# Optimization experiments

Hardware: AMD Instinct MI355X
Metric: run time of the kernel (lower is better)

## Reference

```python
import jax, jax.numpy as jnp
import numpy as np

N, D, E = 50000, 64, 800000  # nodes, node_dim, edges


def setup_inputs() -> dict:
    key = jax.random.key(0)
    ks = jax.random.split(key, 9)
    def lin(kw, fan_in, fan_out):
        # torch nn.Linear default init: U(-1/sqrt(fan_in), 1/sqrt(fan_in))
        bound = 1.0 / np.sqrt(fan_in)
        kw1, kw2 = jax.random.split(kw)
        W = jax.random.uniform(kw1, (fan_in, fan_out), jnp.float32, -bound, bound)
        b = jax.random.uniform(kw2, (fan_out,), jnp.float32, -bound, bound)
        return W, b
    W1, b1 = lin(ks[0], 2 * D + 2, D)
    W2, b2 = lin(ks[1], D, D // 2)
    W3, b3 = lin(ks[2], D // 2, D // 4)
    return {
        "node_features": jax.random.normal(ks[3], (N, D), jnp.float32),
        "edge_index": jax.random.randint(ks[4], (2, E), 0, N, jnp.int64),
        "spatial_features": jax.random.normal(ks[5], (E, 2), jnp.float32),
        "W1": W1, "b1": b1, "W2": W2, "b2": b2, "W3": W3, "b3": b3,
    }


def reference(node_features, edge_index, spatial_features, W1, b1, W2, b2, W3, b3):
    src = node_features[edge_index[0]]          # [E, D] gather
    dst = node_features[edge_index[1]]          # [E, D] gather
    x = jnp.concatenate([src, dst, spatial_features], axis=1)  # [E, 2D+2]
    h = jax.nn.relu(x @ W1 + b1)                # [E, D]
    h = jax.nn.relu(h @ W2 + b2)                # [E, D//2]
    return h @ W3 + b3                          # [E, D//4]
```

## Files before the change

kernel.cpp:

```cpp
#include <hip/hip_runtime.h>
#include <hip/hip_bf16.h>

#define NE 800000
#define NN 50000
#define TPW 5
#define NTILES (NE / 16)
#define NODE_TILES (NN / 16)
#define W1STR 136

typedef __attribute__((ext_vector_type(8))) short        s16x8;
typedef __attribute__((ext_vector_type(4))) short        s16x4;
typedef __attribute__((ext_vector_type(8))) __bf16       bf16x8;
typedef __attribute__((ext_vector_type(4))) __bf16       bf16x4;
typedef __attribute__((ext_vector_type(4))) float        f32x4;
typedef __attribute__((ext_vector_type(2))) float        f32x2;
typedef __attribute__((ext_vector_type(4))) unsigned int u32x4;
typedef __attribute__((ext_vector_type(2))) unsigned int u32x2;

#define TAB_OFF 16384
#define WS_TAB ((size_t)(TAB_OFF + 2ull * NN * 64) * 2)
#define WS_NFB ((size_t)(TAB_OFF + 1ull * NN * 64) * 2)

__device__ __forceinline__ unsigned short f2bf_bits(float f) {
    __bf16 b = (__bf16)f;
    return __builtin_bit_cast(unsigned short, b);
}

__device__ __forceinline__ unsigned int pkbf(float a, float b) {
    return (unsigned int)f2bf_bits(a) | ((unsigned int)f2bf_bits(b) << 16);
}

__device__ __forceinline__ s16x8 cvt8(f32x4 a, f32x4 b) {
    bf16x8 r;
    r[0] = (__bf16)a[0]; r[1] = (__bf16)a[1]; r[2] = (__bf16)a[2]; r[3] = (__bf16)a[3];
    r[4] = (__bf16)b[0]; r[5] = (__bf16)b[1]; r[6] = (__bf16)b[2]; r[7] = (__bf16)b[3];
    return __builtin_bit_cast(s16x8, r);
}

__device__ __forceinline__ int w1addr(int k, int j) {
    return j * W1STR + (((k >> 3) ^ ((j >> 2) & 15)) << 3) + (k & 7);
}

__global__ __launch_bounds__(256) void node_prep_all(
    const float* __restrict__ nf, const float* __restrict__ W1,
    const float* __restrict__ b1, const float* __restrict__ W2,
    const float* __restrict__ W3, unsigned short* __restrict__ ws) {
    unsigned short* w2t = ws + 10240;
    unsigned short* w3t = ws + 12288;
    unsigned short* At  = ws + TAB_OFF;
    unsigned short* Bt  = At + (size_t)NN * 64;

    __shared__ unsigned short w1l[64 * W1STR];

    const int tid = threadIdx.x, wid = tid >> 6, lane = tid & 63;
    const int lr = lane & 15, lg = lane >> 4;

    #pragma unroll
    for (int it = 0; it < 8; ++it) {
        const int i = it * 1024 + tid * 4;
        const int k = i >> 6, j0 = i & 63;
        f32x4 v = *reinterpret_cast<const f32x4*>(W1 + i);
        #pragma unroll
        for (int q = 0; q < 4; ++q)
            w1l[w1addr(k, j0 + q)] = f2bf_bits(v[q]);
    }
    __syncthreads();

    if (blockIdx.x == 0) {
        for (int i = tid; i < 32 * 64; i += 256) {
            int j = i / 64, k = i % 64;
            w2t[i] = f2bf_bits(W2[k * 32 + j]);
        }
        for (int i = tid; i < 16 * 32; i += 256) {
            int j = i / 32, k = i % 32;
            w3t[i] = f2bf_bits(W3[k * 16 + j]);
        }
    }

    s16x8 w1f[4][4];
    #pragma unroll
    for (int s = 0; s < 4; ++s)
        #pragma unroll
        for (int c = 0; c < 4; ++c)
            w1f[s][c] = *reinterpret_cast<const s16x8*>(
                &w1l[w1addr(s * 32 + lg * 8, c * 16 + lr)]);

    f32x4 b1q[4];
    #pragma unroll
    for (int c = 0; c < 4; ++c)
        b1q[c] = *reinterpret_cast<const f32x4*>(b1 + c * 16 + lg * 4);

    const int tile = blockIdx.x * 4 + wid;
    if (tile >= NODE_TILES) return;

    const int row = tile * 16 + lr;
    const float* p = nf + (long)row * 64;
    s16x8 nfr[2];
    #pragma unroll
    for (int s = 0; s < 2; ++s) {
        f32x4 a = *reinterpret_cast<const f32x4*>(p + s * 32 + lg * 8);
        f32x4 b = *reinterpret_cast<const f32x4*>(p + s * 32 + lg * 8 + 4);
        nfr[s] = cvt8(a, b);
    }
    f32x4 a4[4], b4[4];
    #pragma unroll
    for (int c = 0; c < 4; ++c) { a4[c] = (f32x4){0,0,0,0}; b4[c] = (f32x4){0,0,0,0}; }
    #pragma unroll
    for (int s = 0; s < 2; ++s)
        #pragma unroll
        for (int c = 0; c < 4; ++c) {
            a4[c] = __builtin_amdgcn_mfma_f32_16x16x32_bf16(w1f[s][c],     nfr[s], a4[c], 0, 0, 0);
            b4[c] = __builtin_amdgcn_mfma_f32_16x16x32_bf16(w1f[s + 2][c], nfr[s], b4[c], 0, 0, 0);
        }
    #pragma unroll
    for (int c = 0; c < 4; ++c) {
        u32x2 pa, pb;
        pa[0] = pkbf(a4[c][0] + b1q[c][0], a4[c][1] + b1q[c][1]);
        pa[1] = pkbf(a4[c][2] + b1q[c][2], a4[c][3] + b1q[c][3]);
        pb[0] = pkbf(b4[c][0], b4[c][1]);
        pb[1] = pkbf(b4[c][2], b4[c][3]);
        *reinterpret_cast<u32x2*>(At + (long)row * 64 + c * 16 + lg * 4) = pa;
        *reinterpret_cast<u32x2*>(Bt + (long)row * 64 + c * 16 + lg * 4) = pb;
    }
}

__device__ __forceinline__ void gatherT(const unsigned short* At, const unsigned short* Bt,
                                        int si, int di, int lg, s16x8 g[4]) {
    const unsigned short* pa = At + (size_t)si * 64 + lg * 8;
    const unsigned short* pb = Bt + (size_t)di * 64 + lg * 8;
    g[0] = *reinterpret_cast<const s16x8*>(pa);
    g[1] = *reinterpret_cast<const s16x8*>(pa + 32);
    g[2] = *reinterpret_cast<const s16x8*>(pb);
    g[3] = *reinterpret_cast<const s16x8*>(pb + 32);
}

__device__ __forceinline__ void compute_tile(
    int tile, const s16x8 cur[4], f32x2 s2,
    const f32x2 c0p[2][4], const f32x2 c1p[2][4],
    const s16x8 w2f[2][2], s16x8 w3f,
    const f32x4 b2v[2], f32x4 b3v,
    unsigned short* h2w, int lg, int lr, float* __restrict__ out) {

    const f32x2 sp0v = {s2[0], s2[0]}, sp1v = {s2[1], s2[1]};

    s16x8 bfr[2];
    #pragma unroll
    for (int jb = 0; jb < 2; ++jb) {
        u32x4 au = __builtin_bit_cast(u32x4, cur[jb]);
        u32x4 bu = __builtin_bit_cast(u32x4, cur[2 + jb]);
        u32x4 pk4;
        #pragma unroll
        for (int q = 0; q < 4; ++q) {
            f32x2 av = {__builtin_bit_cast(float, au[q] << 16),
                        __builtin_bit_cast(float, au[q] & 0xFFFF0000u)};
            f32x2 bv = {__builtin_bit_cast(float, bu[q] << 16),
                        __builtin_bit_cast(float, bu[q] & 0xFFFF0000u)};
            f32x2 h = av + bv;
            h = sp1v * c1p[jb][q] + h;
            h = sp0v * c0p[jb][q] + h;
            pk4[q] = pkbf(fmaxf(h[0], 0.f), fmaxf(h[1], 0.f));
        }
        bfr[jb] = __builtin_bit_cast(s16x8, pk4);
    }

    f32x4 acc2[2];
    #pragma unroll
    for (int c = 0; c < 2; ++c) acc2[c] = (f32x4){0, 0, 0, 0};
    #pragma unroll
    for (int s = 0; s < 2; ++s)
        #pragma unroll
        for (int c = 0; c < 2; ++c)
            acc2[c] = __builtin_amdgcn_mfma_f32_16x16x32_bf16(w2f[s][c], bfr[s], acc2[c], 0, 0, 0);

    #pragma unroll
    for (int c = 0; c < 2; ++c) {
        u32x2 p;
        p[0] = pkbf(fmaxf(acc2[c][0] + b2v[c][0], 0.f), fmaxf(acc2[c][1] + b2v[c][1], 0.f));
        p[1] = pkbf(fmaxf(acc2[c][2] + b2v[c][2], 0.f), fmaxf(acc2[c][3] + b2v[c][3], 0.f));
        *reinterpret_cast<u32x2*>(h2w + c * 16 + lg * 4) = p;
    }

    s16x8 bf3 = *reinterpret_cast<const s16x8*>(h2w + lg * 8);
    f32x4 acc3 = (f32x4){0, 0, 0, 0};
    acc3 = __builtin_amdgcn_mfma_f32_16x16x32_bf16(w3f, bf3, acc3, 0, 0, 0);

    f32x4 o;
    #pragma unroll
    for (int r = 0; r < 4; ++r) o[r] = acc3[r] + b3v[r];
    __builtin_nontemporal_store(o,
        reinterpret_cast<f32x4*>(out + (long)(tile * 16 + lr) * 16 + lg * 4));
}

__global__ __launch_bounds__(256) void edge_mlp_tab(
    const int* __restrict__ ei, const float* __restrict__ sp,
    const float* __restrict__ W1, const float* __restrict__ b2,
    const float* __restrict__ b3, const unsigned short* __restrict__ wsw,
    float* __restrict__ out) {

    const unsigned short* w2t = wsw + 10240;
    const unsigned short* w3t = wsw + 12288;
    const unsigned short* At  = wsw + TAB_OFF;
    const unsigned short* Bt  = At + (size_t)NN * 64;

    __shared__ unsigned short h2s[4 * 16 * 40];

    const int tid = threadIdx.x, wid = tid >> 6, lane = tid & 63;
    const int lr = lane & 15, lg = lane >> 4;

    const int tile0 = (blockIdx.x * 4 + wid) * TPW;

    s16x8 w2f[2][2], w3f;
    #pragma unroll
    for (int s = 0; s < 2; ++s)
        #pragma unroll
        for (int c = 0; c < 2; ++c)
            w2f[s][c] = *reinterpret_cast<const s16x8*>(w2t + (c * 16 + lr) * 64 + s * 32 + lg * 8);
    w3f = *reinterpret_cast<const s16x8*>(w3t + lr * 32 + lg * 8);

    f32x4 b2v[2];
    #pragma unroll
    for (int c = 0; c < 2; ++c) b2v[c] = *reinterpret_cast<const f32x4*>(b2 + c * 16 + lg * 4);
    const f32x4 b3v = *reinterpret_cast<const f32x4*>(b3 + lg * 4);

    f32x2 c0p[2][4], c1p[2][4];
    #pragma unroll
    for (int jb = 0; jb < 2; ++jb) {
        const int j0 = jb * 32 + lg * 8;
        f32x4 x0 = *reinterpret_cast<const f32x4*>(W1 + 128 * 64 + j0);
        f32x4 x1 = *reinterpret_cast<const f32x4*>(W1 + 128 * 64 + j0 + 4);
        f32x4 y0 = *reinterpret_cast<const f32x4*>(W1 + 129 * 64 + j0);
        f32x4 y1 = *reinterpret_cast<const f32x4*>(W1 + 129 * 64 + j0 + 4);
        c0p[jb][0] = (f32x2){x0[0], x0[1]}; c0p[jb][1] = (f32x2){x0[2], x0[3]};
        c0p[jb][2] = (f32x2){x1[0], x1[1]}; c0p[jb][3] = (f32x2){x1[2], x1[3]};
        c1p[jb][0] = (f32x2){y0[0], y0[1]}; c1p[jb][1] = (f32x2){y0[2], y0[3]};
        c1p[jb][2] = (f32x2){y1[0], y1[1]}; c1p[jb][3] = (f32x2){y1[2], y1[3]};
    }

    unsigned short* h2w = h2s + wid * (16 * 40) + lr * 40;

    int si[TPW], di[TPW];
    f32x2 spv[TPW];
    #pragma unroll
    for (int t = 0; t < TPW; ++t) {
        const size_t e = (size_t)(tile0 + t) * 16 + lr;
        si[t] = ei[e];
        di[t] = ei[NE + e];
        spv[t] = *reinterpret_cast<const f32x2*>(sp + 2 * e);
    }

    s16x8 gA[4], gB[4], gC[4];
    gatherT(At, Bt, si[0], di[0], lg, gA);
    gatherT(At, Bt, si[1], di[1], lg, gB);

    gatherT(At, Bt, si[2], di[2], lg, gC);
    compute_tile(tile0 + 0, gA, spv[0], c0p, c1p, w2f, w3f, b2v, b3v, h2w, lg, lr, out);

    gatherT(At, Bt, si[3], di[3], lg, gA);
    compute_tile(tile0 + 1, gB, spv[1], c0p, c1p, w2f, w3f, b2v, b3v, h2w, lg, lr, out);

    gatherT(At, Bt, si[4], di[4], lg, gB);
    compute_tile(tile0 + 2, gC, spv[2], c0p, c1p, w2f, w3f, b2v, b3v, h2w, lg, lr, out);

    compute_tile(tile0 + 3, gA, spv[3], c0p, c1p, w2f, w3f, b2v, b3v, h2w, lg, lr, out);
    compute_tile(tile0 + 4, gB, spv[4], c0p, c1p, w2f, w3f, b2v, b3v, h2w, lg, lr, out);
}

__global__ void prep(const float* __restrict__ W1, const float* __restrict__ W2,
                     const float* __restrict__ W3, const float* __restrict__ nf,
                     unsigned short* __restrict__ ws, int do_nf) {
    unsigned short* w1t = ws;
    unsigned short* w2t = ws + 10240;
    unsigned short* w3t = ws + 12288;
    int t = blockIdx.x * blockDim.x + threadIdx.x;
    int stride = gridDim.x * blockDim.x;
    for (int i = t; i < 64 * 160; i += stride) {
        int j = i / 160, k = i % 160;
        w1t[i] = f2bf_bits(k < 130 ? W1[k * 64 + j] : 0.0f);
    }
    for (int i = t; i < 32 * 64; i += stride) {
        int j = i / 64, k = i % 64;
        w2t[i] = f2bf_bits(W2[k * 32 + j]);
    }
    for (int i = t; i < 16 * 32; i += stride) {
        int j = i / 32, k = i % 32;
        w3t[i] = f2bf_bits(W3[k * 16 + j]);
    }
    if (do_nf) {
        unsigned short* nfb = ws + TAB_OFF;
        for (int i = t; i < NN * 8; i += stride) {
            f32x4 a = *reinterpret_cast<const f32x4*>(nf + (long)i * 8);
            f32x4 b = *reinterpret_cast<const f32x4*>(nf + (long)i * 8 + 4);
            *reinterpret_cast<s16x8*>(nfb + (long)i * 8) = cvt8(a, b);
        }
    }
}

template <bool BF16NF>
__device__ __forceinline__ void gather4(const unsigned short* nfb, const float* nf,
                                        int si, int di, int lg, s16x8 g[4]) {
    if (BF16NF) {
        #pragma unroll
        for (int s = 0; s < 4; ++s) {
            const int row = (s < 2) ? si : di;
            g[s] = *reinterpret_cast<const s16x8*>(nfb + (long)row * 64 + (s & 1) * 32 + lg * 8);
        }
    } else {
        #pragma unroll
        for (int s = 0; s < 4; ++s) {
            const float* p = nf + (long)((s < 2) ? si : di) * 64 + (s & 1) * 32 + lg * 8;
            f32x4 a = *reinterpret_cast<const f32x4*>(p);
            f32x4 b = *reinterpret_cast<const f32x4*>(p + 4);
            g[s] = cvt8(a, b);
        }
    }
}

template <bool BF16NF>
__global__ __launch_bounds__(256) void edge_mlp_fb(
    const float* __restrict__ nf, const int* __restrict__ ei,
    const float* __restrict__ sp, const float* __restrict__ b1,
    const float* __restrict__ b2, const float* __restrict__ b3,
    const unsigned short* __restrict__ wsw, float* __restrict__ out) {

    const unsigned short* w1t = wsw;
    const unsigned short* w2t = wsw + 10240;
    const unsigned short* w3t = wsw + 12288;
    const unsigned short* nfb = wsw + TAB_OFF;

    __shared__ float h1s[4][16][68];
    __shared__ float h2s[4][16][36];

    const int tid = threadIdx.x, wid = tid >> 6, lane = tid & 63;
    const int lr = lane & 15, lg = lane >> 4;

    s16x8 w1f[5][4], w2f[2][2], w3f;
    #pragma unroll
    for (int s = 0; s < 5; ++s)
        #pragma unroll
        for (int c = 0; c < 4; ++c)
            w1f[s][c] = *reinterpret_cast<const s16x8*>(w1t + (c * 16 + lr) * 160 + s * 32 + lg * 8);
    #pragma unroll
    for (int s = 0; s < 2; ++s)
        #pragma unroll
        for (int c = 0; c < 2; ++c)
            w2f[s][c] = *reinterpret_cast<const s16x8*>(w2t + (c * 16 + lr) * 64 + s * 32 + lg * 8);
    w3f = *reinterpret_cast<const s16x8*>(w3t + lr * 32 + lg * 8);

    float bias1[4], bias2[2], bias3;
    #pragma unroll
    for (int c = 0; c < 4; ++c) bias1[c] = b1[c * 16 + lr];
    #pragma unroll
    for (int c = 0; c < 2; ++c) bias2[c] = b2[c * 16 + lr];
    bias3 = b3[lr];

    const int tile0 = (blockIdx.x * 4 + wid) * 4;
    int si[4], di[4];
    f32x2 spv[4];
    #pragma unroll
    for (int t = 0; t < 4; ++t) {
        const int e = (tile0 + t) * 16 + lr;
        si[t] = ei[e];
        di[t] = ei[NE + e];
        spv[t] = *reinterpret_cast<const f32x2*>(sp + 2 * (size_t)e);
    }

    s16x8 cur[4], nxt[4];
    gather4<BF16NF>(nfb, nf, si[0], di[0], lg, cur);

    #pragma unroll
    for (int tt = 0; tt < 4; ++tt) {
        if (tt + 1 < 4)
            gather4<BF16NF>(nfb, nf, si[tt + 1], di[tt + 1], lg, nxt);

        const int ebase = (tile0 + tt) * 16;

        f32x4 acc1[4];
        #pragma unroll
        for (int c = 0; c < 4; ++c) acc1[c] = (f32x4){0, 0, 0, 0};
        #pragma unroll
        for (int s = 0; s < 4; ++s)
            #pragma unroll
            for (int c = 0; c < 4; ++c)
                acc1[c] = __builtin_amdgcn_mfma_f32_16x16x32_bf16(cur[s], w1f[s][c], acc1[c], 0, 0, 0);
        {
            bf16x8 z;
            #pragma unroll
            for (int j = 0; j < 8; ++j) z[j] = (__bf16)0.0f;
            if (lg == 0) { z[0] = (__bf16)spv[tt][0]; z[1] = (__bf16)spv[tt][1]; }
            s16x8 af = __builtin_bit_cast(s16x8, z);
            #pragma unroll
            for (int c = 0; c < 4; ++c)
                acc1[c] = __builtin_amdgcn_mfma_f32_16x16x32_bf16(af, w1f[4][c], acc1[c], 0, 0, 0);
        }
        #pragma unroll
        for (int c = 0; c < 4; ++c)
            #pragma unroll
            for (int r = 0; r < 4; ++r)
                h1s[wid][lg * 4 + r][c * 16 + lr] = fmaxf(acc1[c][r] + bias1[c], 0.0f);

        f32x4 acc2[2];
        #pragma unroll
        for (int c = 0; c < 2; ++c) acc2[c] = (f32x4){0, 0, 0, 0};
        #pragma unroll
        for (int s = 0; s < 2; ++s) {
            f32x4 a = *reinterpret_cast<const f32x4*>(&h1s[wid][lr][s * 32 + lg * 8]);
            f32x4 b = *reinterpret_cast<const f32x4*>(&h1s[wid][lr][s * 32 + lg * 8 + 4]);
            s16x8 af = cvt8(a, b);
            #pragma unroll
            for (int c = 0; c < 2; ++c)
                acc2[c] = __builtin_amdgcn_mfma_f32_16x16x32_bf16(af, w2f[s][c], acc2[c], 0, 0, 0);
        }
        #pragma unroll
        for (int c = 0; c < 2; ++c)
            #pragma unroll
            for (int r = 0; r < 4; ++r)
                h2s[wid][lg * 4 + r][c * 16 + lr] = fmaxf(acc2[c][r] + bias2[c], 0.0f);

        f32x4 a3 = *reinterpret_cast<const f32x4*>(&h2s[wid][lr][lg * 8]);
        f32x4 b3x = *reinterpret_cast<const f32x4*>(&h2s[wid][lr][lg * 8 + 4]);
        s16x8 af3 = cvt8(a3, b3x);
        f32x4 acc3 = (f32x4){0, 0, 0, 0};
        acc3 = __builtin_amdgcn_mfma_f32_16x16x32_bf16(af3, w3f, acc3, 0, 0, 0);
        #pragma unroll
        for (int r = 0; r < 4; ++r)
            out[(long)(ebase + lg * 4 + r) * 16 + lr] = acc3[r] + bias3;

        #pragma unroll
        for (int s = 0; s < 4; ++s) cur[s] = nxt[s];
    }
}

extern "C" void kernel_launch(void* const* d_in, const int* in_sizes, int n_in,
                              void* d_out, int out_size, void* d_ws, size_t ws_size,
                              hipStream_t stream) {
    const float* nf = (const float*)d_in[0];
    const int*   ei = (const int*)d_in[1];
    const float* sp = (const float*)d_in[2];
    const float* W1 = (const float*)d_in[3];
    const float* b1 = (const float*)d_in[4];
    const float* W2 = (const float*)d_in[5];
    const float* b2 = (const float*)d_in[6];
    const float* W3 = (const float*)d_in[7];
    const float* b3 = (const float*)d_in[8];
    float* out = (float*)d_out;
    unsigned short* wsw = (unsigned short*)d_ws;

    const bool tab  = (ws_size >= WS_TAB);
    const bool bnfb = (!tab && ws_size >= WS_NFB);

    if (tab) {
        const int pblocks = (NODE_TILES + 3) / 4;
        hipLaunchKernelGGL(node_prep_all, dim3(pblocks), dim3(256), 0, stream,
                           nf, W1, b1, W2, W3, wsw);
        const int blocks = NTILES / (TPW * 4);
        hipLaunchKernelGGL(edge_mlp_tab, dim3(blocks), dim3(256), 0, stream,
                           ei, sp, W1, b2, b3, wsw, out);
    } else {
        hipLaunchKernelGGL(prep, dim3(64), dim3(256), 0, stream,
                           W1, W2, W3, nf, wsw, bnfb ? 1 : 0);
        const int blocks = NTILES / 4 / 4;
        if (bnfb)
            hipLaunchKernelGGL(edge_mlp_fb<true>, dim3(blocks), dim3(256), 0, stream,
                               nf, ei, sp, b1, b2, b3, wsw, out);
        else
            hipLaunchKernelGGL(edge_mlp_fb<false>, dim3(blocks), dim3(256), 0, stream,
                               nf, ei, sp, b1, b2, b3, wsw, out);
    }
}
```

Measured before the change: 57.08 us.

## Fuse node prep and edge MLP into one cooperative persistent kernel

Combines the node-table precompute and the edge MLP into a single cooperative kernel of 2048 blocks that uses a grid-wide sync between the two phases. This removes one kernel launch and the gap between launches. It also switches the edge phase to a persistent layout of 6 tiles per wave, with a tail tile for some waves and triple-buffered gathers. The cost is a grid barrier, occupancy checks on the host on every call, and register pressure from launch bounds of 8 blocks per CU.

```diff
diff --git a/kernel.cpp b/kernel.cpp
--- a/kernel.cpp
+++ b/kernel.cpp
@@ -1,5 +1,8 @@
 #include <hip/hip_runtime.h>
 #include <hip/hip_bf16.h>
+#include <hip/hip_cooperative_groups.h>
+
+namespace cg = cooperative_groups;
 
 #define NE 800000
 #define NN 50000
@@ -8,10 +11,13 @@
 #define NODE_TILES (NN / 16)
 #define W1STR 136
 
+#define FBLOCKS 2048
+#define FWAVES  (FBLOCKS * 4)
+#define FTPW    6
+#define FTAIL   (NTILES - FWAVES * FTPW)
+
 typedef __attribute__((ext_vector_type(8))) short        s16x8;
-typedef __attribute__((ext_vector_type(4))) short        s16x4;
 typedef __attribute__((ext_vector_type(8))) __bf16       bf16x8;
-typedef __attribute__((ext_vector_type(4))) __bf16       bf16x4;
 typedef __attribute__((ext_vector_type(4))) float        f32x4;
 typedef __attribute__((ext_vector_type(2))) float        f32x2;
 typedef __attribute__((ext_vector_type(4))) unsigned int u32x4;
@@ -39,89 +45,6 @@
 
 __device__ __forceinline__ int w1addr(int k, int j) {
     return j * W1STR + (((k >> 3) ^ ((j >> 2) & 15)) << 3) + (k & 7);
-}
-
-__global__ __launch_bounds__(256) void node_prep_all(
-    const float* __restrict__ nf, const float* __restrict__ W1,
-    const float* __restrict__ b1, const float* __restrict__ W2,
-    const float* __restrict__ W3, unsigned short* __restrict__ ws) {
-    unsigned short* w2t = ws + 10240;
-    unsigned short* w3t = ws + 12288;
-    unsigned short* At  = ws + TAB_OFF;
-    unsigned short* Bt  = At + (size_t)NN * 64;
-
-    __shared__ unsigned short w1l[64 * W1STR];
-
-    const int tid = threadIdx.x, wid = tid >> 6, lane = tid & 63;
-    const int lr = lane & 15, lg = lane >> 4;
-
-    #pragma unroll
-    for (int it = 0; it < 8; ++it) {
-        const int i = it * 1024 + tid * 4;
-        const int k = i >> 6, j0 = i & 63;
-        f32x4 v = *reinterpret_cast<const f32x4*>(W1 + i);
-        #pragma unroll
-        for (int q = 0; q < 4; ++q)
-            w1l[w1addr(k, j0 + q)] = f2bf_bits(v[q]);
-    }
-    __syncthreads();
-
-    if (blockIdx.x == 0) {
-        for (int i = tid; i < 32 * 64; i += 256) {
-            int j = i / 64, k = i % 64;
-            w2t[i] = f2bf_bits(W2[k * 32 + j]);
-        }
-        for (int i = tid; i < 16 * 32; i += 256) {
-            int j = i / 32, k = i % 32;
-            w3t[i] = f2bf_bits(W3[k * 16 + j]);
-        }
-    }
-
-    s16x8 w1f[4][4];
-    #pragma unroll
-    for (int s = 0; s < 4; ++s)
-        #pragma unroll
-        for (int c = 0; c < 4; ++c)
-            w1f[s][c] = *reinterpret_cast<const s16x8*>(
-                &w1l[w1addr(s * 32 + lg * 8, c * 16 + lr)]);
-
-    f32x4 b1q[4];
-    #pragma unroll
-    for (int c = 0; c < 4; ++c)
-        b1q[c] = *reinterpret_cast<const f32x4*>(b1 + c * 16 + lg * 4);
-
-    const int tile = blockIdx.x * 4 + wid;
-    if (tile >= NODE_TILES) return;
-
-    const int row = tile * 16 + lr;
-    const float* p = nf + (long)row * 64;
-    s16x8 nfr[2];
-    #pragma unroll
-    for (int s = 0; s < 2; ++s) {
-        f32x4 a = *reinterpret_cast<const f32x4*>(p + s * 32 + lg * 8);
-        f32x4 b = *reinterpret_cast<const f32x4*>(p + s * 32 + lg * 8 + 4);
-        nfr[s] = cvt8(a, b);
-    }
-    f32x4 a4[4], b4[4];
-    #pragma unroll
-    for (int c = 0; c < 4; ++c) { a4[c] = (f32x4){0,0,0,0}; b4[c] = (f32x4){0,0,0,0}; }
-    #pragma unroll
-    for (int s = 0; s < 2; ++s)
-        #pragma unroll
-        for (int c = 0; c < 4; ++c) {
-            a4[c] = __builtin_amdgcn_mfma_f32_16x16x32_bf16(w1f[s][c],     nfr[s], a4[c], 0, 0, 0);
-            b4[c] = __builtin_amdgcn_mfma_f32_16x16x32_bf16(w1f[s + 2][c], nfr[s], b4[c], 0, 0, 0);
-        }
-    #pragma unroll
-    for (int c = 0; c < 4; ++c) {
-        u32x2 pa, pb;
-        pa[0] = pkbf(a4[c][0] + b1q[c][0], a4[c][1] + b1q[c][1]);
-        pa[1] = pkbf(a4[c][2] + b1q[c][2], a4[c][3] + b1q[c][3]);
-        pb[0] = pkbf(b4[c][0], b4[c][1]);
-        pb[1] = pkbf(b4[c][2], b4[c][3]);
-        *reinterpret_cast<u32x2*>(At + (long)row * 64 + c * 16 + lg * 4) = pa;
-        *reinterpret_cast<u32x2*>(Bt + (long)row * 64 + c * 16 + lg * 4) = pb;
-    }
 }
 
 __device__ __forceinline__ void gatherT(const unsigned short* At, const unsigned short* Bt,
@@ -189,6 +112,251 @@
     for (int r = 0; r < 4; ++r) o[r] = acc3[r] + b3v[r];
     __builtin_nontemporal_store(o,
         reinterpret_cast<f32x4*>(out + (long)(tile * 16 + lr) * 16 + lg * 4));
+}
+
+__global__ __launch_bounds__(256, 8) void fused_all(
+    const float* __restrict__ nf, const int* __restrict__ ei,
+    const float* __restrict__ sp, const float* __restrict__ W1,
+    const float* __restrict__ b1, const float* __restrict__ W2,
+    const float* __restrict__ b2, const float* __restrict__ W3,
+    const float* __restrict__ b3, unsigned short* __restrict__ ws,
+    float* __restrict__ out) {
+
+    unsigned short* w2t = ws + 10240;
+    unsigned short* w3t = ws + 12288;
+    unsigned short* At  = ws + TAB_OFF;
+    unsigned short* Bt  = At + (size_t)NN * 64;
+
+    __shared__ unsigned short smem[64 * W1STR];
+
+    const int tid = threadIdx.x, wid = tid >> 6, lane = tid & 63;
+    const int lr = lane & 15, lg = lane >> 4;
+    const int gw = blockIdx.x * 4 + wid;
+
+    if (blockIdx.x < (NODE_TILES + 3) / 4) {
+        #pragma unroll
+        for (int it = 0; it < 8; ++it) {
+            const int i = it * 1024 + tid * 4;
+            const int k = i >> 6, j0 = i & 63;
+            f32x4 v = *reinterpret_cast<const f32x4*>(W1 + i);
+            #pragma unroll
+            for (int q = 0; q < 4; ++q)
+                smem[w1addr(k, j0 + q)] = f2bf_bits(v[q]);
+        }
+        __syncthreads();
+
+        if (blockIdx.x == 0) {
+            for (int i = tid; i < 32 * 64; i += 256) {
+                int j = i / 64, k = i % 64;
+                w2t[i] = f2bf_bits(W2[k * 32 + j]);
+            }
+            for (int i = tid; i < 16 * 32; i += 256) {
+                int j = i / 32, k = i % 32;
+                w3t[i] = f2bf_bits(W3[k * 16 + j]);
+            }
+        }
+
+        s16x8 w1f[4][4];
+        #pragma unroll
+        for (int s = 0; s < 4; ++s)
+            #pragma unroll
+            for (int c = 0; c < 4; ++c)
+                w1f[s][c] = *reinterpret_cast<const s16x8*>(
+                    &smem[w1addr(s * 32 + lg * 8, c * 16 + lr)]);
+
+        if (gw < NODE_TILES) {
+            f32x4 b1q[4];
+            #pragma unroll
+            for (int c = 0; c < 4; ++c)
+                b1q[c] = *reinterpret_cast<const f32x4*>(b1 + c * 16 + lg * 4);
+
+            const int row = gw * 16 + lr;
+            const float* p = nf + (long)row * 64;
+            s16x8 nfr[2];
+            #pragma unroll
+            for (int s = 0; s < 2; ++s) {
+                f32x4 a = *reinterpret_cast<const f32x4*>(p + s * 32 + lg * 8);
+                f32x4 b = *reinterpret_cast<const f32x4*>(p + s * 32 + lg * 8 + 4);
+                nfr[s] = cvt8(a, b);
+            }
+            f32x4 a4[4], b4[4];
+            #pragma unroll
+            for (int c = 0; c < 4; ++c) { a4[c] = (f32x4){0,0,0,0}; b4[c] = (f32x4){0,0,0,0}; }
+            #pragma unroll
+            for (int s = 0; s < 2; ++s)
+                #pragma unroll
+                for (int c = 0; c < 4; ++c) {
+                    a4[c] = __builtin_amdgcn_mfma_f32_16x16x32_bf16(w1f[s][c],     nfr[s], a4[c], 0, 0, 0);
+                    b4[c] = __builtin_amdgcn_mfma_f32_16x16x32_bf16(w1f[s + 2][c], nfr[s], b4[c], 0, 0, 0);
+                }
+            #pragma unroll
+            for (int c = 0; c < 4; ++c) {
+                u32x2 pa, pb;
+                pa[0] = pkbf(a4[c][0] + b1q[c][0], a4[c][1] + b1q[c][1]);
+                pa[1] = pkbf(a4[c][2] + b1q[c][2], a4[c][3] + b1q[c][3]);
+                pb[0] = pkbf(b4[c][0], b4[c][1]);
+                pb[1] = pkbf(b4[c][2], b4[c][3]);
+                *reinterpret_cast<u32x2*>(At + (long)row * 64 + c * 16 + lg * 4) = pa;
+                *reinterpret_cast<u32x2*>(Bt + (long)row * 64 + c * 16 + lg * 4) = pb;
+            }
+        }
+    }
+
+    __threadfence();
+    cg::this_grid().sync();
+
+    s16x8 w2f[2][2], w3f;
+    #pragma unroll
+    for (int s = 0; s < 2; ++s)
+        #pragma unroll
+        for (int c = 0; c < 2; ++c)
+            w2f[s][c] = *reinterpret_cast<const s16x8*>(w2t + (c * 16 + lr) * 64 + s * 32 + lg * 8);
+    w3f = *reinterpret_cast<const s16x8*>(w3t + lr * 32 + lg * 8);
+
+    f32x4 b2v[2];
+    #pragma unroll
+    for (int c = 0; c < 2; ++c) b2v[c] = *reinterpret_cast<const f32x4*>(b2 + c * 16 + lg * 4);
+    const f32x4 b3v = *reinterpret_cast<const f32x4*>(b3 + lg * 4);
+
+    f32x2 c0p[2][4], c1p[2][4];
+    #pragma unroll
+    for (int jb = 0; jb < 2; ++jb) {
+        const int j0 = jb * 32 + lg * 8;
+        f32x4 x0 = *reinterpret_cast<const f32x4*>(W1 + 128 * 64 + j0);
+        f32x4 x1 = *reinterpret_cast<const f32x4*>(W1 + 128 * 64 + j0 + 4);
+        f32x4 y0 = *reinterpret_cast<const f32x4*>(W1 + 129 * 64 + j0);
+        f32x4 y1 = *reinterpret_cast<const f32x4*>(W1 + 129 * 64 + j0 + 4);
+        c0p[jb][0] = (f32x2){x0[0], x0[1]}; c0p[jb][1] = (f32x2){x0[2], x0[3]};
+        c0p[jb][2] = (f32x2){x1[0], x1[1]}; c0p[jb][3] = (f32x2){x1[2], x1[3]};
+        c1p[jb][0] = (f32x2){y0[0], y0[1]}; c1p[jb][1] = (f32x2){y0[2], y0[3]};
+        c1p[jb][2] = (f32x2){y1[0], y1[1]}; c1p[jb][3] = (f32x2){y1[2], y1[3]};
+    }
+
+    unsigned short* h2w = smem + wid * (16 * 40) + lr * 40;
+
+    const bool extra = (gw < FTAIL);
+    const int tile0 = gw * FTPW + (extra ? gw : FTAIL);
+
+    int si[FTPW], di[FTPW];
+    f32x2 spv[FTPW];
+    #pragma unroll
+    for (int t = 0; t < FTPW; ++t) {
+        const size_t e = (size_t)(tile0 + t) * 16 + lr;
+        si[t] = ei[e];
+        di[t] = ei[NE + e];
+        spv[t] = *reinterpret_cast<const f32x2*>(sp + 2 * e);
+    }
+
+    s16x8 gA[4], gB[4], gC[4];
+    gatherT(At, Bt, si[0], di[0], lg, gA);
+    gatherT(At, Bt, si[1], di[1], lg, gB);
+
+    gatherT(At, Bt, si[2], di[2], lg, gC);
+    compute_tile(tile0 + 0, gA, spv[0], c0p, c1p, w2f, w3f, b2v, b3v, h2w, lg, lr, out);
+
+    gatherT(At, Bt, si[3], di[3], lg, gA);
+    compute_tile(tile0 + 1, gB, spv[1], c0p, c1p, w2f, w3f, b2v, b3v, h2w, lg, lr, out);
+
+    gatherT(At, Bt, si[4], di[4], lg, gB);
+    compute_tile(tile0 + 2, gC, spv[2], c0p, c1p, w2f, w3f, b2v, b3v, h2w, lg, lr, out);
+
+    gatherT(At, Bt, si[5], di[5], lg, gC);
+    compute_tile(tile0 + 3, gA, spv[3], c0p, c1p, w2f, w3f, b2v, b3v, h2w, lg, lr, out);
+
+    compute_tile(tile0 + 4, gB, spv[4], c0p, c1p, w2f, w3f, b2v, b3v, h2w, lg, lr, out);
+    compute_tile(tile0 + 5, gC, spv[5], c0p, c1p, w2f, w3f, b2v, b3v, h2w, lg, lr, out);
+
+    if (extra) {
+        const int t6 = tile0 + 6;
+        const size_t e = (size_t)t6 * 16 + lr;
+        const int s6 = ei[e], d6 = ei[NE + e];
+        const f32x2 p6 = *reinterpret_cast<const f32x2*>(sp + 2 * e);
+        gatherT(At, Bt, s6, d6, lg, gA);
+        compute_tile(t6, gA, p6, c0p, c1p, w2f, w3f, b2v, b3v, h2w, lg, lr, out);
+    }
+}
+
+__global__ __launch_bounds__(256) void node_prep_all(
+    const float* __restrict__ nf, const float* __restrict__ W1,
+    const float* __restrict__ b1, const float* __restrict__ W2,
+    const float* __restrict__ W3, unsigned short* __restrict__ ws) {
+    unsigned short* w2t = ws + 10240;
+    unsigned short* w3t = ws + 12288;
+    unsigned short* At  = ws + TAB_OFF;
+    unsigned short* Bt  = At + (size_t)NN * 64;
+
+    __shared__ unsigned short w1l[64 * W1STR];
+
+    const int tid = threadIdx.x, wid = tid >> 6, lane = tid & 63;
+    const int lr = lane & 15, lg = lane >> 4;
+
+    #pragma unroll
+    for (int it = 0; it < 8; ++it) {
+        const int i = it * 1024 + tid * 4;
+        const int k = i >> 6, j0 = i & 63;
+        f32x4 v = *reinterpret_cast<const f32x4*>(W1 + i);
+        #pragma unroll
+        for (int q = 0; q < 4; ++q)
+            w1l[w1addr(k, j0 + q)] = f2bf_bits(v[q]);
+    }
+    __syncthreads();
+
+    if (blockIdx.x == 0) {
+        for (int i = tid; i < 32 * 64; i += 256) {
+            int j = i / 64, k = i % 64;
+            w2t[i] = f2bf_bits(W2[k * 32 + j]);
+        }
+        for (int i = tid; i < 16 * 32; i += 256) {
+            int j = i / 32, k = i % 32;
+            w3t[i] = f2bf_bits(W3[k * 16 + j]);
+        }
+    }
+
+    s16x8 w1f[4][4];
+    #pragma unroll
+    for (int s = 0; s < 4; ++s)
+        #pragma unroll
+        for (int c = 0; c < 4; ++c)
+            w1f[s][c] = *reinterpret_cast<const s16x8*>(
+                &w1l[w1addr(s * 32 + lg * 8, c * 16 + lr)]);
+
+    f32x4 b1q[4];
+    #pragma unroll
+    for (int c = 0; c < 4; ++c)
+        b1q[c] = *reinterpret_cast<const f32x4*>(b1 + c * 16 + lg * 4);
+
+    const int tile = blockIdx.x * 4 + wid;
+    if (tile >= NODE_TILES) return;
+
+    const int row = tile * 16 + lr;
+    const float* p = nf + (long)row * 64;
+    s16x8 nfr[2];
+    #pragma unroll
+    for (int s = 0; s < 2; ++s) {
+        f32x4 a = *reinterpret_cast<const f32x4*>(p + s * 32 + lg * 8);
+        f32x4 b = *reinterpret_cast<const f32x4*>(p + s * 32 + lg * 8 + 4);
+        nfr[s] = cvt8(a, b);
+    }
+    f32x4 a4[4], b4[4];
+    #pragma unroll
+    for (int c = 0; c < 4; ++c) { a4[c] = (f32x4){0,0,0,0}; b4[c] = (f32x4){0,0,0,0}; }
+    #pragma unroll
+    for (int s = 0; s < 2; ++s)
+        #pragma unroll
+        for (int c = 0; c < 4; ++c) {
+            a4[c] = __builtin_amdgcn_mfma_f32_16x16x32_bf16(w1f[s][c],     nfr[s], a4[c], 0, 0, 0);
+            b4[c] = __builtin_amdgcn_mfma_f32_16x16x32_bf16(w1f[s + 2][c], nfr[s], b4[c], 0, 0, 0);
+        }
+    #pragma unroll
+    for (int c = 0; c < 4; ++c) {
+        u32x2 pa, pb;
+        pa[0] = pkbf(a4[c][0] + b1q[c][0], a4[c][1] + b1q[c][1]);
+        pa[1] = pkbf(a4[c][2] + b1q[c][2], a4[c][3] + b1q[c][3]);
+        pb[0] = pkbf(b4[c][0], b4[c][1]);
+        pb[1] = pkbf(b4[c][2], b4[c][3]);
+        *reinterpret_cast<u32x2*>(At + (long)row * 64 + c * 16 + lg * 4) = pa;
+        *reinterpret_cast<u32x2*>(Bt + (long)row * 64 + c * 16 + lg * 4) = pb;
+    }
 }
 
 __global__ __launch_bounds__(256) void edge_mlp_tab(
@@ -449,12 +617,27 @@
     const bool bnfb = (!tab && ws_size >= WS_NFB);
 
     if (tab) {
-        const int pblocks = (NODE_TILES + 3) / 4;
-        hipLaunchKernelGGL(node_prep_all, dim3(pblocks), dim3(256), 0, stream,
-                           nf, W1, b1, W2, W3, wsw);
-        const int blocks = NTILES / (TPW * 4);
-        hipLaunchKernelGGL(edge_mlp_tab, dim3(blocks), dim3(256), 0, stream,
-                           ei, sp, W1, b2, b3, wsw, out);
+        bool done = false;
+        int maxb = 0, ncu = 0;
+        if (hipOccupancyMaxActiveBlocksPerMultiprocessor(
+                &maxb, (const void*)fused_all, 256, 0) == hipSuccess &&
+            hipDeviceGetAttribute(&ncu, hipDeviceAttributeMultiprocessorCount, 0)
+                == hipSuccess && (long)maxb * ncu >= FBLOCKS) {
+            void* args[] = {(void*)&nf, (void*)&ei, (void*)&sp, (void*)&W1,
+                            (void*)&b1, (void*)&W2, (void*)&b2, (void*)&W3,
+                            (void*)&b3, (void*)&wsw, (void*)&out};
+            hipError_t le = hipLaunchCooperativeKernel(
+                (const void*)fused_all, dim3(FBLOCKS), dim3(256), args, 0, stream);
+            done = (le == hipSuccess);
+        }
+        if (!done) {
+            const int pblocks = (NODE_TILES + 3) / 4;
+            hipLaunchKernelGGL(node_prep_all, dim3(pblocks), dim3(256), 0, stream,
+                               nf, W1, b1, W2, W3, wsw);
+            const int blocks = NTILES / (TPW * 4);
+            hipLaunchKernelGGL(edge_mlp_tab, dim3(blocks), dim3(256), 0, stream,
+                               ei, sp, W1, b2, b3, wsw, out);
+        }
     } else {
         hipLaunchKernelGGL(prep, dim3(64), dim3(256), 0, stream,
                            W1, W2, W3, nf, wsw, bnfb ? 1 : 0);
```

Result: no change. 56.98 us (-0.2%).
